# Kernel tuning notes

Hardware: AMD Instinct MI355X
Metric: run time of the kernel (lower is better)

## Reference

```python
import jax, jax.numpy as jnp
import numpy as np

FLOAT_MIN = np.float32(np.finfo(np.float32).min)  # torch.finfo().min for float32
K_DIM = 64  # init kwarg, equals head dim of query/key


def setup_inputs() -> dict:
    key = jax.random.key(0)
    k1, k2, k3, k4 = jax.random.split(key, 4)
    B, Lq, Lk, D, Dv = 16, 2048, 2048, 64, 64
    return {
        "query": jax.random.normal(k1, (B, Lq, D), dtype=jnp.float32),
        "key": jax.random.normal(k2, (B, Lk, D), dtype=jnp.float32),
        "value": jax.random.normal(k3, (B, Lk, Dv), dtype=jnp.float32),
        "mask": jax.random.uniform(k4, (1, Lq, Lk), dtype=jnp.float32),
    }


def reference(query, key, value, mask):
    # scores: [B, Lq, Lk]
    scores = jnp.einsum("bqd,bkd->bqk", query, key) / jnp.sqrt(jnp.float32(K_DIM))
    # multiplicative mask -> additive log-bias, clamped at float32 min
    scores = scores + jnp.maximum(jnp.log(mask), FLOAT_MIN)
    # NOTE: source applies softmax over dim=1 (the query axis), faithfully reproduced
    attn = jax.nn.softmax(scores, axis=1)
    return jnp.einsum("bqk,bkv->bqv", attn, value)
```

## Files before the change

kernel.cpp:

```cpp
#include <hip/hip_runtime.h>
#include <cstdint>
#include <cstddef>


#define LSEQ 2048
#define DHEAD 64

typedef __bf16 v8bf __attribute__((ext_vector_type(8)));
typedef __bf16 v4bf __attribute__((ext_vector_type(4)));
typedef float v4f __attribute__((ext_vector_type(4)));

#define MFMA16(a, b, c) __builtin_amdgcn_mfma_f32_16x16x32_bf16(a, b, c, 0, 0, 0)

__device__ __forceinline__ void gl_lds16(const void* g, void* l) {
  __builtin_amdgcn_global_load_lds(
      (__attribute__((address_space(1))) void*)g,
      (__attribute__((address_space(3))) void*)l, 16, 0, 0);
}

__global__ __launch_bounds__(256) void cast_qk(const float* __restrict__ Q,
                                               const float* __restrict__ K,
                                               __bf16* __restrict__ Qb,
                                               __bf16* __restrict__ Kb) {
  size_t i = ((size_t)blockIdx.x * 256 + threadIdx.x) * 4;
  float4 q = *(const float4*)(Q + i);
  float4 k = *(const float4*)(K + i);
  v4bf qo = {(__bf16)q.x, (__bf16)q.y, (__bf16)q.z, (__bf16)q.w};
  v4bf ko = {(__bf16)k.x, (__bf16)k.y, (__bf16)k.z, (__bf16)k.w};
  *(v4bf*)(Qb + i) = qo;
  *(v4bf*)(Kb + i) = ko;
}

__global__ __launch_bounds__(256) void stats_k(const __bf16* __restrict__ Qb,
                                               const __bf16* __restrict__ Kb,
                                               const float* __restrict__ mask,
                                               float* __restrict__ Lsum) {
  const int bx = blockIdx.x;
  const int b = bx >> 7;
  const int qc = (bx >> 5) & 3;
  const int k0 = (bx & 31) * 64;
  const int tid = threadIdx.x;
  const int wave = tid >> 6, lane = tid & 63;
  const int quad = lane >> 4, n = lane & 15;

  __shared__ __align__(16) __bf16 Qt[64 * 64];
  __shared__ float psum[4][64];

  v8bf bk[4][2];
#pragma unroll
  for (int sub = 0; sub < 4; ++sub)
#pragma unroll
    for (int dh = 0; dh < 2; ++dh)
      bk[sub][dh] = *(const v8bf*)(Kb + ((size_t)b * LSEQ + k0 + sub * 16 + n) * DHEAD +
                                   dh * 32 + quad * 8);

  float colsum[4] = {0.f, 0.f, 0.f, 0.f};

  const int qbeg = qc * 512;
  for (int q0 = qbeg; q0 < qbeg + 512; q0 += 64) {
    __syncthreads();
#pragma unroll
    for (int i = 0; i < 2; ++i) {
      int s = (wave * 2 + i) * 64 + lane;
      int row = s >> 3, gc = (s & 7) ^ (row & 7);
      gl_lds16(Qb + ((size_t)b * LSEQ + q0 + row) * DHEAD + gc * 8, &Qt[s * 8]);
    }
    __syncthreads();

    v8bf aq[2];
    const int qr = wave * 16 + n;
#pragma unroll
    for (int dh = 0; dh < 2; ++dh)
      aq[dh] = *(const v8bf*)&Qt[qr * 64 + ((dh * 4 + quad) ^ (qr & 7)) * 8];

#pragma unroll
    for (int sub = 0; sub < 4; ++sub) {
      v4f c = {0.f, 0.f, 0.f, 0.f};
      c = MFMA16(aq[0], bk[sub][0], c);
      c = MFMA16(aq[1], bk[sub][1], c);
      const int kg = k0 + sub * 16 + n;
#pragma unroll
      for (int r = 0; r < 4; ++r) {
        int qg = q0 + wave * 16 + quad * 4 + r;
        float p = mask[(size_t)qg * LSEQ + kg] * __expf(c[r] * 0.125f);
        colsum[sub] += p;
      }
    }
  }

#pragma unroll
  for (int sub = 0; sub < 4; ++sub) {
    float v = colsum[sub];
    v += __shfl_xor(v, 16);
    v += __shfl_xor(v, 32);
    if (quad == 0) psum[wave][sub * 16 + n] = v;
  }
  __syncthreads();
  if (tid < 64) {
    float s = psum[0][tid] + psum[1][tid] + psum[2][tid] + psum[3][tid];
    unsafeAtomicAdd(&Lsum[(size_t)b * LSEQ + k0 + tid], s);
  }
}

__global__ __launch_bounds__(256) void vtrans_k(const float* __restrict__ V,
                                                const float* __restrict__ Lsum,
                                                __bf16* __restrict__ Vts) {
  const int b = blockIdx.x >> 6;
  const int k0 = (blockIdx.x & 63) * 32;
  const int tid = threadIdx.x;
  __shared__ float tile[32][65];
  __shared__ float invl[32];
  if (tid < 32) invl[tid] = 1.0f / Lsum[(size_t)b * LSEQ + k0 + tid];
#pragma unroll
  for (int t = 0; t < 8; ++t) {
    int flat = t * 256 + tid;
    int k = flat >> 6, v = flat & 63;
    tile[k][v] = V[((size_t)b * LSEQ + k0 + k) * DHEAD + v];
  }
  __syncthreads();
#pragma unroll
  for (int t = 0; t < 8; ++t) {
    int flat = t * 256 + tid;
    int v = flat >> 5, k = flat & 31;
    Vts[((size_t)b * DHEAD + v) * LSEQ + k0 + k] = (__bf16)(tile[k][v] * invl[k]);
  }
}

__global__ __launch_bounds__(256) void attn_k(const __bf16* __restrict__ Qb,
                                              const __bf16* __restrict__ Kb,
                                              const __bf16* __restrict__ Vts,
                                              const float* __restrict__ mask,
                                              float* __restrict__ out) {
  const int bx = blockIdx.x;
  const int b = bx >> 7;
  const int kc = (bx >> 5) & 3;
  const int q0 = (bx & 31) * 64;
  const int tid = threadIdx.x;
  const int wave = tid >> 6, lane = tid & 63;
  const int quad = lane >> 4, n = lane & 15;

  __shared__ __align__(16) __bf16 Kt[64 * 64];
  __shared__ __align__(16) __bf16 Vt[64 * 64];
  __shared__ __align__(16) __bf16 Pt[64 * 72];

  v8bf aq[2];
  {
    const int qr = q0 + wave * 16 + n;
#pragma unroll
    for (int dh = 0; dh < 2; ++dh)
      aq[dh] = *(const v8bf*)(Qb + ((size_t)b * LSEQ + qr) * DHEAD + dh * 32 + quad * 8);
  }

  v4f acc[4];
#pragma unroll
  for (int vs = 0; vs < 4; ++vs) acc[vs] = (v4f){0.f, 0.f, 0.f, 0.f};

  const int kbeg = kc * 512;
  for (int k0 = kbeg; k0 < kbeg + 512; k0 += 64) {
    __syncthreads();
#pragma unroll
    for (int i = 0; i < 2; ++i) {
      int s = (wave * 2 + i) * 64 + lane;
      int row = s >> 3, gc = (s & 7) ^ (row & 7);
      gl_lds16(Kb + ((size_t)b * LSEQ + k0 + row) * DHEAD + gc * 8, &Kt[s * 8]);
      gl_lds16(Vts + ((size_t)b * DHEAD + row) * LSEQ + k0 + gc * 8, &Vt[s * 8]);
    }
    __syncthreads();

#pragma unroll
    for (int sub = 0; sub < 4; ++sub) {
      v4f c = {0.f, 0.f, 0.f, 0.f};
      const int kr = sub * 16 + n;
#pragma unroll
      for (int dh = 0; dh < 2; ++dh) {
        v8bf bkf = *(const v8bf*)&Kt[kr * 64 + ((dh * 4 + quad) ^ (kr & 7)) * 8];
        c = MFMA16(aq[dh], bkf, c);
      }
      const int kg = k0 + kr;
#pragma unroll
      for (int r = 0; r < 4; ++r) {
        int qg = q0 + wave * 16 + quad * 4 + r;
        float p = mask[(size_t)qg * LSEQ + kg] * __expf(c[r] * 0.125f);
        Pt[(wave * 16 + quad * 4 + r) * 72 + kr] = (__bf16)p;
      }
    }
    __asm__ volatile("s_waitcnt lgkmcnt(0)" ::: "memory");

#pragma unroll
    for (int kk = 0; kk < 2; ++kk) {
      v8bf ap = *(const v8bf*)&Pt[(wave * 16 + n) * 72 + kk * 32 + quad * 8];
#pragma unroll
      for (int vs = 0; vs < 4; ++vs) {
        const int vr = vs * 16 + n;
        v8bf bv = *(const v8bf*)&Vt[vr * 64 + ((kk * 4 + quad) ^ (vr & 7)) * 8];
        acc[vs] = MFMA16(ap, bv, acc[vs]);
      }
    }
  }

#pragma unroll
  for (int vs = 0; vs < 4; ++vs)
#pragma unroll
    for (int r = 0; r < 4; ++r)
      unsafeAtomicAdd(
          &out[((size_t)b * LSEQ + q0 + wave * 16 + quad * 4 + r) * DHEAD + vs * 16 + n],
          acc[vs][r]);
}

extern "C" void kernel_launch(void* const* d_in, const int* in_sizes, int n_in,
                              void* d_out, int out_size, void* d_ws, size_t ws_size,
                              hipStream_t stream) {
  const float* Q = (const float*)d_in[0];
  const float* K = (const float*)d_in[1];
  const float* V = (const float*)d_in[2];
  const float* mask = (const float*)d_in[3];
  float* out = (float*)d_out;

  char* ws = (char*)d_ws;
  __bf16* Qb = (__bf16*)(ws);
  __bf16* Kb = (__bf16*)(ws + 4194304);
  __bf16* Vts = (__bf16*)(ws + 8388608);
  float* Lsum = (float*)(ws + 12582912);
  if (ws_size < 12713984) return;

  hipMemsetAsync(Lsum, 0, LSEQ * 16 * sizeof(float), stream);
  hipMemsetAsync(out, 0, (size_t)out_size * sizeof(float), stream);
  cast_qk<<<2048, 256, 0, stream>>>(Q, K, Qb, Kb);
  stats_k<<<2048, 256, 0, stream>>>(Qb, Kb, mask, Lsum);
  vtrans_k<<<1024, 256, 0, stream>>>(V, Lsum, Vts);
  attn_k<<<2048, 256, 0, stream>>>(Qb, Kb, Vts, mask, out);
}
```

Before: 170.4 us.

## Transpose MFMA operands for vectorized mask loads, fold scale into Q, drop atomics

Swaps the MFMA A/B operands so each lane holds four consecutive key columns for one query row. The mask can then be read as float4 and P written as a packed v4bf, replacing scattered scalar accesses. The softmax scale and log2(e) are folded into Q during the bf16 cast so exp2 can be used directly. Column sums are written as per-chunk partials into the output buffer instead of atomically added to a memset workspace, with the output memset moved after the transpose kernel.

```diff
diff --git a/kernel.cpp b/kernel.cpp
--- a/kernel.cpp
+++ b/kernel.cpp
@@ -11,6 +11,12 @@
 typedef float v4f __attribute__((ext_vector_type(4)));
 
 #define MFMA16(a, b, c) __builtin_amdgcn_mfma_f32_16x16x32_bf16(a, b, c, 0, 0, 0)
+
+#if __has_builtin(__builtin_amdgcn_exp2f)
+#define EXP2F(x) __builtin_amdgcn_exp2f(x)
+#else
+#define EXP2F(x) __expf((x) * 0.6931471805599453f)
+#endif
 
 __device__ __forceinline__ void gl_lds16(const void* g, void* l) {
   __builtin_amdgcn_global_load_lds(
@@ -22,10 +28,11 @@
                                                const float* __restrict__ K,
                                                __bf16* __restrict__ Qb,
                                                __bf16* __restrict__ Kb) {
+  const float S = 0.18033688011112042f;
   size_t i = ((size_t)blockIdx.x * 256 + threadIdx.x) * 4;
   float4 q = *(const float4*)(Q + i);
   float4 k = *(const float4*)(K + i);
-  v4bf qo = {(__bf16)q.x, (__bf16)q.y, (__bf16)q.z, (__bf16)q.w};
+  v4bf qo = {(__bf16)(q.x * S), (__bf16)(q.y * S), (__bf16)(q.z * S), (__bf16)(q.w * S)};
   v4bf ko = {(__bf16)k.x, (__bf16)k.y, (__bf16)k.z, (__bf16)k.w};
   *(v4bf*)(Qb + i) = qo;
   *(v4bf*)(Kb + i) = ko;
@@ -34,7 +41,7 @@
 __global__ __launch_bounds__(256) void stats_k(const __bf16* __restrict__ Qb,
                                                const __bf16* __restrict__ Kb,
                                                const float* __restrict__ mask,
-                                               float* __restrict__ Lsum) {
+                                               float* __restrict__ Lpart) {
   const int bx = blockIdx.x;
   const int b = bx >> 7;
   const int qc = (bx >> 5) & 3;
@@ -44,17 +51,21 @@
   const int quad = lane >> 4, n = lane & 15;
 
   __shared__ __align__(16) __bf16 Qt[64 * 64];
-  __shared__ float psum[4][64];
-
-  v8bf bk[4][2];
+  __shared__ __align__(16) float psum[4][64];
+
+  v8bf ak[4][2];
 #pragma unroll
   for (int sub = 0; sub < 4; ++sub)
 #pragma unroll
     for (int dh = 0; dh < 2; ++dh)
-      bk[sub][dh] = *(const v8bf*)(Kb + ((size_t)b * LSEQ + k0 + sub * 16 + n) * DHEAD +
+      ak[sub][dh] = *(const v8bf*)(Kb + ((size_t)b * LSEQ + k0 + sub * 16 + n) * DHEAD +
                                    dh * 32 + quad * 8);
 
-  float colsum[4] = {0.f, 0.f, 0.f, 0.f};
+  float colsum[4][4];
+#pragma unroll
+  for (int s = 0; s < 4; ++s)
+#pragma unroll
+    for (int r = 0; r < 4; ++r) colsum[s][r] = 0.f;
 
   const int qbeg = qc * 512;
   for (int q0 = qbeg; q0 < qbeg + 512; q0 += 64) {
@@ -67,50 +78,60 @@
     }
     __syncthreads();
 
-    v8bf aq[2];
+    v8bf bq[2];
     const int qr = wave * 16 + n;
 #pragma unroll
     for (int dh = 0; dh < 2; ++dh)
-      aq[dh] = *(const v8bf*)&Qt[qr * 64 + ((dh * 4 + quad) ^ (qr & 7)) * 8];
+      bq[dh] = *(const v8bf*)&Qt[qr * 64 + ((dh * 4 + quad) ^ (qr & 7)) * 8];
 
 #pragma unroll
     for (int sub = 0; sub < 4; ++sub) {
       v4f c = {0.f, 0.f, 0.f, 0.f};
-      c = MFMA16(aq[0], bk[sub][0], c);
-      c = MFMA16(aq[1], bk[sub][1], c);
-      const int kg = k0 + sub * 16 + n;
-#pragma unroll
-      for (int r = 0; r < 4; ++r) {
-        int qg = q0 + wave * 16 + quad * 4 + r;
-        float p = mask[(size_t)qg * LSEQ + kg] * __expf(c[r] * 0.125f);
-        colsum[sub] += p;
-      }
+      c = MFMA16(ak[sub][0], bq[0], c);
+      c = MFMA16(ak[sub][1], bq[1], c);
+      const float4 m4 = *(const float4*)&mask[(size_t)(q0 + wave * 16 + n) * LSEQ +
+                                              k0 + sub * 16 + quad * 4];
+#pragma unroll
+      for (int r = 0; r < 4; ++r)
+        colsum[sub][r] += ((const float*)&m4)[r] * EXP2F(c[r]);
     }
   }
 
 #pragma unroll
   for (int sub = 0; sub < 4; ++sub) {
-    float v = colsum[sub];
-    v += __shfl_xor(v, 16);
-    v += __shfl_xor(v, 32);
-    if (quad == 0) psum[wave][sub * 16 + n] = v;
+#pragma unroll
+    for (int r = 0; r < 4; ++r) {
+      float v = colsum[sub][r];
+      v += __shfl_xor(v, 1);
+      v += __shfl_xor(v, 2);
+      v += __shfl_xor(v, 4);
+      v += __shfl_xor(v, 8);
+      colsum[sub][r] = v;
+    }
+    if (n == 0) {
+      v4f w = {colsum[sub][0], colsum[sub][1], colsum[sub][2], colsum[sub][3]};
+      *(v4f*)&psum[wave][sub * 16 + quad * 4] = w;
+    }
   }
   __syncthreads();
   if (tid < 64) {
     float s = psum[0][tid] + psum[1][tid] + psum[2][tid] + psum[3][tid];
-    unsafeAtomicAdd(&Lsum[(size_t)b * LSEQ + k0 + tid], s);
+    Lpart[((size_t)b * LSEQ + k0 + tid) * 4 + qc] = s;
   }
 }
 
 __global__ __launch_bounds__(256) void vtrans_k(const float* __restrict__ V,
-                                                const float* __restrict__ Lsum,
+                                                const float* __restrict__ Lpart,
                                                 __bf16* __restrict__ Vts) {
   const int b = blockIdx.x >> 6;
   const int k0 = (blockIdx.x & 63) * 32;
   const int tid = threadIdx.x;
   __shared__ float tile[32][65];
   __shared__ float invl[32];
-  if (tid < 32) invl[tid] = 1.0f / Lsum[(size_t)b * LSEQ + k0 + tid];
+  if (tid < 32) {
+    float4 lp = *(const float4*)&Lpart[((size_t)b * LSEQ + k0 + tid) * 4];
+    invl[tid] = 1.0f / (lp.x + lp.y + lp.z + lp.w);
+  }
 #pragma unroll
   for (int t = 0; t < 8; ++t) {
     int flat = t * 256 + tid;
@@ -143,12 +164,12 @@
   __shared__ __align__(16) __bf16 Vt[64 * 64];
   __shared__ __align__(16) __bf16 Pt[64 * 72];
 
-  v8bf aq[2];
+  v8bf bq[2];
   {
     const int qr = q0 + wave * 16 + n;
 #pragma unroll
     for (int dh = 0; dh < 2; ++dh)
-      aq[dh] = *(const v8bf*)(Qb + ((size_t)b * LSEQ + qr) * DHEAD + dh * 32 + quad * 8);
+      bq[dh] = *(const v8bf*)(Qb + ((size_t)b * LSEQ + qr) * DHEAD + dh * 32 + quad * 8);
   }
 
   v4f acc[4];
@@ -173,16 +194,16 @@
       const int kr = sub * 16 + n;
 #pragma unroll
       for (int dh = 0; dh < 2; ++dh) {
-        v8bf bkf = *(const v8bf*)&Kt[kr * 64 + ((dh * 4 + quad) ^ (kr & 7)) * 8];
-        c = MFMA16(aq[dh], bkf, c);
+        v8bf akf = *(const v8bf*)&Kt[kr * 64 + ((dh * 4 + quad) ^ (kr & 7)) * 8];
+        c = MFMA16(akf, bq[dh], c);
       }
-      const int kg = k0 + kr;
-#pragma unroll
-      for (int r = 0; r < 4; ++r) {
-        int qg = q0 + wave * 16 + quad * 4 + r;
-        float p = mask[(size_t)qg * LSEQ + kg] * __expf(c[r] * 0.125f);
-        Pt[(wave * 16 + quad * 4 + r) * 72 + kr] = (__bf16)p;
-      }
+      const float4 m4 = *(const float4*)&mask[(size_t)(q0 + wave * 16 + n) * LSEQ +
+                                              k0 + sub * 16 + quad * 4];
+      v4bf pw;
+#pragma unroll
+      for (int r = 0; r < 4; ++r)
+        pw[r] = (__bf16)(((const float*)&m4)[r] * EXP2F(c[r]));
+      *(v4bf*)&Pt[(wave * 16 + n) * 72 + sub * 16 + quad * 4] = pw;
     }
     __asm__ volatile("s_waitcnt lgkmcnt(0)" ::: "memory");
 
@@ -220,13 +241,12 @@
   __bf16* Qb = (__bf16*)(ws);
   __bf16* Kb = (__bf16*)(ws + 4194304);
   __bf16* Vts = (__bf16*)(ws + 8388608);
-  float* Lsum = (float*)(ws + 12582912);
-  if (ws_size < 12713984) return;
-
-  hipMemsetAsync(Lsum, 0, LSEQ * 16 * sizeof(float), stream);
+  float* Lpart = (float*)d_out;
+  if (ws_size < 12582912) return;
+
+  cast_qk<<<2048, 256, 0, stream>>>(Q, K, Qb, Kb);
+  stats_k<<<2048, 256, 0, stream>>>(Qb, Kb, mask, Lpart);
+  vtrans_k<<<1024, 256, 0, stream>>>(V, Lpart, Vts);
   hipMemsetAsync(out, 0, (size_t)out_size * sizeof(float), stream);
-  cast_qk<<<2048, 256, 0, stream>>>(Q, K, Qb, Kb);
-  stats_k<<<2048, 256, 0, stream>>>(Qb, Kb, mask, Lsum);
-  vtrans_k<<<1024, 256, 0, stream>>>(V, Lsum, Vts);
   attn_k<<<2048, 256, 0, stream>>>(Qb, Kb, Vts, mask, out);
 }
```

New measurement: 212.6 us. 1.25x slower.
